# Optimization experiments

Hardware: AMD Instinct MI355X
Metric: run time of the kernel (lower is better)

The kernel has to match this reference:

```python
import jax, jax.numpy as jnp
import numpy as np

B, T, E = 4, 2048, 1024
H, D = 16, 64  # num_heads, head_size; H*D == E


def setup_inputs() -> dict:
    key = jax.random.key(0)
    ks = jax.random.split(key, 8)
    s = 0.02
    x = jax.random.normal(ks[0], (B, T, E), dtype=jnp.float32)
    attention_mask = jnp.ones((B, T), dtype=jnp.float32)
    # stacked per-head projection weights (no bias), torch Linear: y = x @ W.T
    Wq = jax.random.normal(ks[1], (H, E, D), dtype=jnp.float32) * s
    Wk = jax.random.normal(ks[2], (H, E, D), dtype=jnp.float32) * s
    Wv = jax.random.normal(ks[3], (H, E, D), dtype=jnp.float32) * s
    Wo = jax.random.normal(ks[4], (E, E), dtype=jnp.float32) * s
    bo = jnp.zeros((E,), dtype=jnp.float32)
    return {"x": x, "attention_mask": attention_mask, "Wq": Wq, "Wk": Wk,
            "Wv": Wv, "Wo": Wo, "bo": bo}


def reference(x, attention_mask, Wq, Wk, Wv, Wo, bo):
    # per-head projections, vectorized over heads: [B,T,E] x [H,E,D] -> [B,H,T,D]
    q = jnp.einsum('bte,hed->bhtd', x, Wq)
    k = jnp.einsum('bte,hed->bhtd', x, Wk)
    v = jnp.einsum('bte,hed->bhtd', x, Wv)
    scores = jnp.einsum('bhtd,bhsd->bhts', q, k) / jnp.sqrt(jnp.float32(D))
    # causal mask (tril): masked_fill with -inf
    causal = jnp.tril(jnp.ones((T, T), dtype=bool))
    scores = jnp.where(causal[None, None, :, :], scores, -jnp.inf)
    # padding mask: weights += (1 - mask) * finfo(float32).min, broadcast over queries
    neg = jnp.finfo(jnp.float32).min
    scores = scores + ((1.0 - attention_mask) * neg)[:, None, None, :]
    weights = jax.nn.softmax(scores, axis=-1)
    out = jnp.einsum('bhts,bhsd->bthd', weights, v).reshape(B, T, H * D)
    return out @ Wo.T + bo
```

## Files before the change

kernel.cpp:

```cpp
#include <hip/hip_runtime.h>
#include <hip/hip_bf16.h>

#define B_ 4
#define T_ 2048
#define E_ 1024
#define H_ 16
#define D_ 64
#define M_ (B_*T_)

typedef short bf16x8 __attribute__((ext_vector_type(8)));
typedef float f32x4  __attribute__((ext_vector_type(4)));
typedef float f32x16 __attribute__((ext_vector_type(16)));

__device__ __forceinline__ short f2bf(float f) {
    __hip_bfloat16 h = __float2bfloat16(f);
    return *reinterpret_cast<short*>(&h);
}

__device__ __forceinline__ void async_ld16(const void* g, void* l) {
    __builtin_amdgcn_global_load_lds(
        (const __attribute__((address_space(1))) unsigned int*)g,
        (__attribute__((address_space(3))) unsigned int*)l, 16, 0, 0);
}

__global__ __launch_bounds__(256) void prep_fused(
        const float* __restrict__ x,   const float* __restrict__ Wo,
        const float* __restrict__ Wq,  const float* __restrict__ Wk,
        const float* __restrict__ Wv,  const float* __restrict__ mask,
        short* __restrict__ xb, short* __restrict__ Wob,
        short* __restrict__ Wt, float* __restrict__ bias) {
    __shared__ float tile[64][65];
    const int bi  = blockIdx.x;
    const int tid = threadIdx.x;

    if (bi < 9216) {
        const float* src = (bi < 8192) ? x : Wo;
        short* dst       = (bi < 8192) ? xb : Wob;
        const int i = ((bi < 8192) ? bi : (bi - 8192)) * 256 + tid;
        float4 v = ((const float4*)src)[i];
        short4 o = make_short4(f2bf(v.x), f2bf(v.y), f2bf(v.z), f2bf(v.w));
        ((short4*)dst)[i] = o;
    } else if (bi < 9984) {
        const int idx = bi - 9216;
        const int which = idx >> 8;
        const int h  = (idx & 255) >> 4;
        const int e0 = (idx & 15) * 64;
        const float* __restrict__ W = (which == 0) ? Wq : (which == 1) ? Wk : Wv;
#pragma unroll
        for (int r = 0; r < 4; ++r) {
            int lin = tid + r * 256;
            int er = lin >> 4, c4 = (lin & 15) * 4;
            float4 v = *(const float4*)(W + ((size_t)h * E_ + e0 + er) * D_ + c4);
            tile[er][c4 + 0] = v.x; tile[er][c4 + 1] = v.y;
            tile[er][c4 + 2] = v.z; tile[er][c4 + 3] = v.w;
        }
        __syncthreads();
#pragma unroll
        for (int r = 0; r < 4; ++r) {
            int lin = tid + r * 256;
            int dr = lin >> 4, j4 = (lin & 15) * 4;
            short4 o = make_short4(f2bf(tile[j4 + 0][dr]), f2bf(tile[j4 + 1][dr]),
                                   f2bf(tile[j4 + 2][dr]), f2bf(tile[j4 + 3][dr]));
            *(short4*)(Wt + ((size_t)which * 1024 + h * 64 + dr) * E_ + e0 + j4) = o;
        }
    } else {
        const int i = (bi - 9984) * 256 + tid;
        float bm = (1.0f - mask[i]) * -3.402823466e38f;
        bias[i] = fmaf(bm, 1.4426950f, -8.6561700f);
    }
}

template <int MODE>
__global__ __launch_bounds__(512, 4) void mfma_gemm(
        const short* __restrict__ A,
        const short* __restrict__ Bt,
        short* __restrict__ qo, short* __restrict__ ko, short* __restrict__ vo,
        float* __restrict__ Cout, const float* __restrict__ bo) {
    __shared__ __align__(16) char lds[3 * 24576];

    const int tid  = threadIdx.x;
    const int wave = tid >> 6, lane = tid & 63;
    const int c = lane & 15, quad = lane >> 4;
    const int wm = wave >> 1, wn = wave & 1;
    const int m0 = blockIdx.x * 256;
    const int n0 = blockIdx.y * 128;

    const int ar = tid >> 2;
    const int ag = (tid & 3) ^ ((tid >> 3) & 3);

    int aoff[4], boff[4];
#pragma unroll
    for (int mi = 0; mi < 4; ++mi) {
        int row = wm * 64 + mi * 16 + c;
        aoff[mi] = row * 64 + ((quad ^ ((row >> 1) & 3)) << 4);
    }
#pragma unroll
    for (int ni = 0; ni < 4; ++ni) {
        int row = wn * 64 + ni * 16 + c;
        boff[ni] = 16384 + row * 64 + ((quad ^ ((row >> 1) & 3)) << 4);
    }

    f32x4 acc[4][4] = {};

#define STG(bufb, k0v) do {                                                  \
        async_ld16(A  + (size_t)(m0 + ar) * 1024 + (k0v) + ag * 8,           \
                   lds + (bufb) + wave * 1024);                              \
        async_ld16(A  + (size_t)(m0 + 128 + ar) * 1024 + (k0v) + ag * 8,     \
                   lds + (bufb) + 8192 + wave * 1024);                       \
        async_ld16(Bt + (size_t)(n0 + ar) * 1024 + (k0v) + ag * 8,           \
                   lds + (bufb) + 16384 + wave * 1024);                      \
    } while (0)

    STG(0, 0);
    STG(24576, 32);
    asm volatile("s_waitcnt vmcnt(3)" ::: "memory");
    __builtin_amdgcn_s_barrier();

    int rbase = 0;
#pragma unroll 1
    for (int k = 0; k < 32; ++k) {
        const char* rb = lds + rbase;
        const int wbase = (rbase == 0) ? 49152 : rbase - 24576;

        if (k < 30) STG(wbase, (k + 2) * 32);

        bf16x8 a_[4], b_[4];
#pragma unroll
        for (int mi = 0; mi < 4; ++mi)
            a_[mi] = *(const bf16x8*)(rb + aoff[mi]);
#pragma unroll
        for (int ni = 0; ni < 4; ++ni)
            b_[ni] = *(const bf16x8*)(rb + boff[ni]);

        __builtin_amdgcn_s_setprio(1);
#pragma unroll
        for (int mi = 0; mi < 4; ++mi)
#pragma unroll
            for (int ni = 0; ni < 4; ++ni)
                acc[mi][ni] = __builtin_amdgcn_mfma_f32_16x16x32_bf16(
                    a_[mi], b_[ni], acc[mi][ni], 0, 0, 0);
        __builtin_amdgcn_s_setprio(0);

        if (k < 30)       asm volatile("s_waitcnt vmcnt(3)" ::: "memory");
        else if (k == 30) asm volatile("s_waitcnt vmcnt(0)" ::: "memory");
        if (k < 31) __builtin_amdgcn_s_barrier();

        rbase = (rbase == 49152) ? 0 : rbase + 24576;
    }
#undef STG

    if (MODE == 0) {
        const int which = n0 >> 10;
        const int nb = n0 & 1023;
        if (which == 2) {
#pragma unroll
            for (int mi = 0; mi < 4; ++mi) {
                const int m = m0 + wm * 64 + mi * 16 + quad * 4;
                const int b = m >> 11, t = m & 2047;
#pragma unroll
                for (int ni = 0; ni < 4; ++ni) {
                    const int n = nb + wn * 64 + ni * 16 + c;
                    const int h = n >> 6, d = n & 63;
                    short4 s4 = make_short4(f2bf(acc[mi][ni][0]), f2bf(acc[mi][ni][1]),
                                            f2bf(acc[mi][ni][2]), f2bf(acc[mi][ni][3]));
                    *(short4*)(vo + (((size_t)b * H_ + h) * D_ + d) * T_ + t) = s4;
                }
            }
        } else {
            short* __restrict__ outp = (which == 0) ? qo : ko;
            const float sc = (which == 0) ? 0.18033688f : 1.0f;
#pragma unroll
            for (int mi = 0; mi < 4; ++mi) {
#pragma unroll
                for (int i = 0; i < 4; ++i) {
                    const int m = m0 + wm * 64 + mi * 16 + quad * 4 + i;
                    const int b = m >> 11, t = m & 2047;
#pragma unroll
                    for (int ni = 0; ni < 4; ++ni) {
                        const int n = nb + wn * 64 + ni * 16 + c;
                        const int h = n >> 6, d = n & 63;
                        outp[(((size_t)b * H_ + h) * T_ + t) * D_ + d] =
                            f2bf(acc[mi][ni][i] * sc);
                    }
                }
            }
        }
    } else {
#pragma unroll
        for (int mi = 0; mi < 4; ++mi) {
#pragma unroll
            for (int i = 0; i < 4; ++i) {
                const int m = m0 + wm * 64 + mi * 16 + quad * 4 + i;
#pragma unroll
                for (int ni = 0; ni < 4; ++ni) {
                    const int n = n0 + wn * 64 + ni * 16 + c;
                    Cout[(size_t)m * E_ + n] = acc[mi][ni][i] + bo[n];
                }
            }
        }
    }
}

__global__ __launch_bounds__(256, 4) void flash_attn7(
        const short* __restrict__ qg,
        const short* __restrict__ kg,
        const short* __restrict__ vtg,
        const float* __restrict__ biasg,
        short* __restrict__ attn) {
    const int h = blockIdx.x, b = blockIdx.y;
    const int kb = 15 - blockIdx.z;
    const int tid  = threadIdx.x;
    const int wave = tid >> 6, lane = tid & 63;
    const int ln = lane & 31, hi = lane >> 5;
    const int q0w = kb * 128 + wave * 32;
    const int mytile = 4 * kb + wave;
    const int nt = 4 * kb + 4;

    __shared__ __align__(16) char lds[40960];

    const size_t bh = (size_t)b * H_ + h;
    const short* qbh  = qg  + bh * (size_t)T_ * D_;
    const short* kbh  = kg  + bh * (size_t)T_ * D_;
    const short* vtbh = vtg + bh * (size_t)D_ * T_;
    const float* biasb = biasg + (size_t)b * T_;

    const int ks = tid >> 3, kgs = (tid & 7) ^ (ks & 7);
    const int vd = tid >> 2, vgs = ((tid & 3) - (vd >> 1)) & 3;

    int kaddr[4];
#pragma unroll
    for (int kc = 0; kc < 4; ++kc)
        kaddr[kc] = ln * 128 + ((((kc << 1) + hi) ^ (ln & 7)) << 4);
    int vaddr[4];
#pragma unroll
    for (int dh = 0; dh < 2; ++dh)
#pragma unroll
        for (int kc2 = 0; kc2 < 2; ++kc2) {
            int d = dh * 32 + ln;
            vaddr[dh * 2 + kc2] =
                4096 + d * 64 + (((((kc2 << 1) + hi) + (d >> 1)) & 3) << 4);
        }

    bf16x8 qf[4];
#pragma unroll
    for (int kc = 0; kc < 4; ++kc)
        qf[kc] = *(const bf16x8*)(qbh + (size_t)(q0w + ln) * D_ + kc * 16 + hi * 8);

#pragma unroll
    for (int r = 0; r < 2; ++r)
        async_ld16(biasb + r * 1024 + tid * 4,
                   lds + 32768 + r * 4096 + wave * 1024);

#define STAGE_T(tt2) do {                                                   \
        const int _s0 = (tt2) << 5;                                         \
        const int _bb = ((tt2) & 3) * 8192;                                 \
        async_ld16(kbh + (size_t)(_s0 + ks) * D_ + (kgs << 3),              \
                   lds + _bb + wave * 1024);                                \
        async_ld16(vtbh + (size_t)vd * T_ + _s0 + (vgs << 3),               \
                   lds + _bb + 4096 + wave * 1024);                         \
    } while (0)

    STAGE_T(0);
    STAGE_T(1);

    f32x16 O0 = {}, O1 = {};
    float lacc = 0.0f;

    for (int tt = 0; tt < nt; ++tt) {
        if (tt + 2 < nt) STAGE_T(tt + 2);
        const int rem = nt - 1 - tt;
        if (rem >= 2)      asm volatile("s_waitcnt vmcnt(4)" ::: "memory");
        else if (rem == 1) asm volatile("s_waitcnt vmcnt(2)" ::: "memory");
        else               asm volatile("s_waitcnt vmcnt(0)" ::: "memory");
        __builtin_amdgcn_s_barrier();

        if (tt <= mytile) {
            const int s0 = tt << 5;
            const int bb = (tt & 3) * 8192;

            f32x4 b4[4];
#pragma unroll
            for (int g = 0; g < 4; ++g)
                b4[g] = *(const f32x4*)(lds + 32768 + (s0 + g * 8 + hi * 4) * 4);

            f32x16 S = {};
            __builtin_amdgcn_s_setprio(1);
#pragma unroll
            for (int kc = 0; kc < 4; ++kc) {
                bf16x8 ka = *(const bf16x8*)(lds + bb + kaddr[kc]);
                S = __builtin_amdgcn_mfma_f32_32x32x16_bf16(ka, qf[kc], S, 0, 0, 0);
            }
            __builtin_amdgcn_s_setprio(0);

            float p[16];
#pragma unroll
            for (int r = 0; r < 16; ++r) {
                float bb2 = ((const float*)&b4[r >> 2])[r & 3];
                p[r] = __builtin_amdgcn_exp2f(S[r] + bb2);
            }
            if (tt == mytile) {
#pragma unroll
                for (int r = 0; r < 16; ++r)
                    if (((r & 3) + ((r >> 2) << 3) + (hi << 2)) > ln)
                        p[r] = 0.0f;
            }
            {
                float t0 = (p[0] + p[1]) + (p[2] + p[3]);
                float t1 = (p[4] + p[5]) + (p[6] + p[7]);
                float t2s = (p[8] + p[9]) + (p[10] + p[11]);
                float t3 = (p[12] + p[13]) + (p[14] + p[15]);
                lacc += (t0 + t1) + (t2s + t3);
            }

            unsigned int u0, u1, u2, u3, u4, u5, u6, u7;
            asm("v_cvt_pk_bf16_f32 %0, %1, %2" : "=v"(u0) : "v"(p[0]),  "v"(p[1]));
            asm("v_cvt_pk_bf16_f32 %0, %1, %2" : "=v"(u1) : "v"(p[2]),  "v"(p[3]));
            asm("v_cvt_pk_bf16_f32 %0, %1, %2" : "=v"(u2) : "v"(p[4]),  "v"(p[5]));
            asm("v_cvt_pk_bf16_f32 %0, %1, %2" : "=v"(u3) : "v"(p[6]),  "v"(p[7]));
            asm("v_cvt_pk_bf16_f32 %0, %1, %2" : "=v"(u4) : "v"(p[8]),  "v"(p[9]));
            asm("v_cvt_pk_bf16_f32 %0, %1, %2" : "=v"(u5) : "v"(p[10]), "v"(p[11]));
            asm("v_cvt_pk_bf16_f32 %0, %1, %2" : "=v"(u6) : "v"(p[12]), "v"(p[13]));
            asm("v_cvt_pk_bf16_f32 %0, %1, %2" : "=v"(u7) : "v"(p[14]), "v"(p[15]));
            asm("v_permlane32_swap_b32 %0, %1" : "+v"(u0), "+v"(u2));
            asm("v_permlane32_swap_b32 %0, %1" : "+v"(u1), "+v"(u3));
            asm("v_permlane32_swap_b32 %0, %1" : "+v"(u4), "+v"(u6));
            asm("v_permlane32_swap_b32 %0, %1" : "+v"(u5), "+v"(u7));
            union { unsigned int w[4]; bf16x8 v; } pa0, pa1;
            pa0.w[0] = u0; pa0.w[1] = u1; pa0.w[2] = u2; pa0.w[3] = u3;
            pa1.w[0] = u4; pa1.w[1] = u5; pa1.w[2] = u6; pa1.w[3] = u7;

            bf16x8 v00 = *(const bf16x8*)(lds + bb + vaddr[0]);
            bf16x8 v01 = *(const bf16x8*)(lds + bb + vaddr[1]);
            bf16x8 v10 = *(const bf16x8*)(lds + bb + vaddr[2]);
            bf16x8 v11 = *(const bf16x8*)(lds + bb + vaddr[3]);
            __builtin_amdgcn_s_setprio(1);
            O0 = __builtin_amdgcn_mfma_f32_32x32x16_bf16(pa0.v, v00, O0, 0, 0, 0);
            O0 = __builtin_amdgcn_mfma_f32_32x32x16_bf16(pa1.v, v01, O0, 0, 0, 0);
            O1 = __builtin_amdgcn_mfma_f32_32x32x16_bf16(pa0.v, v10, O1, 0, 0, 0);
            O1 = __builtin_amdgcn_mfma_f32_32x32x16_bf16(pa1.v, v11, O1, 0, 0, 0);
            __builtin_amdgcn_s_setprio(0);
        }
    }
#undef STAGE_T

    unsigned int la = __float_as_uint(lacc), lb2 = la;
    asm("v_permlane32_swap_b32 %0, %1" : "+v"(la), "+v"(lb2));
    const float ltot = __uint_as_float(la) + __uint_as_float(lb2);

    __syncthreads();
    float* lsh = (float*)lds + wave * 32;
    if (hi == 0) lsh[ln] = 1.0f / ltot;
    __syncthreads();

    short* ab = attn + (size_t)b * T_ * E_ + h * D_;
#pragma unroll
    for (int r = 0; r < 16; ++r) {
        const int qrow = (r & 3) + ((r >> 2) << 3) + (hi << 2);
        const float iv = lsh[qrow];
        const size_t base = (size_t)(q0w + qrow) * E_;
        ab[base + ln]      = f2bf(O0[r] * iv);
        ab[base + 32 + ln] = f2bf(O1[r] * iv);
    }
}

extern "C" void kernel_launch(void* const* d_in, const int* in_sizes, int n_in,
                              void* d_out, int out_size, void* d_ws, size_t ws_size,
                              hipStream_t stream) {
    const float* x    = (const float*)d_in[0];
    const float* mask = (const float*)d_in[1];
    const float* Wq   = (const float*)d_in[2];
    const float* Wk   = (const float*)d_in[3];
    const float* Wv   = (const float*)d_in[4];
    const float* Wo   = (const float*)d_in[5];
    const float* bo   = (const float*)d_in[6];
    float* out        = (float*)d_out;

    const size_t S = (size_t)M_ * E_;
    char* ws = (char*)d_ws;
    short* xb   = (short*)ws;
    short* qb   = (short*)(ws + S * 2);
    short* kb   = (short*)(ws + S * 4);
    short* vtb  = (short*)(ws + S * 6);
    short* Wt   = (short*)(ws + S * 8);
    short* Wob  = (short*)(ws + S * 8 + (size_t)3 * 1024 * 1024 * 2);
    float* bias = (float*)(ws + S * 8 + (size_t)4 * 1024 * 1024 * 2);
    short* attnb = xb;

    prep_fused<<<dim3(10016), 256, 0, stream>>>(
        x, Wo, Wq, Wk, Wv, mask, xb, Wob, Wt, bias);

    mfma_gemm<0><<<dim3(M_ / 256, 3 * E_ / 128), 512, 0, stream>>>(
        xb, Wt, qb, kb, vtb, nullptr, nullptr);

    flash_attn7<<<dim3(H_, B_, 16), 256, 0, stream>>>(qb, kb, vtb, bias, attnb);

    mfma_gemm<1><<<dim3(M_ / 256, E_ / 128), 512, 0, stream>>>(
        attnb, Wob, nullptr, nullptr, nullptr, out, bo);
}
```

Before: 234.3 us.

## Process attention KV tiles in pairs with one barrier and swizzle GEMM block order

The flash attention loop now handles two 32-key tiles per iteration. It waits on all outstanding loads and takes one barrier per pair, then prefetches the next pair into the other half of the 4-slot ring. This halves the number of barriers and waitcnts, but drops the finer-grained prefetch overlap of the old two-tile-ahead scheme. Separately, the GEMM kernels remap block indices with an 8-way swizzle, spreading consecutive blocks across XCDs/L2 domains to improve cache locality.

```diff
diff --git a/kernel.cpp b/kernel.cpp
--- a/kernel.cpp
+++ b/kernel.cpp
@@ -82,8 +82,12 @@
     const int wave = tid >> 6, lane = tid & 63;
     const int c = lane & 15, quad = lane >> 4;
     const int wm = wave >> 1, wn = wave & 1;
-    const int m0 = blockIdx.x * 256;
-    const int n0 = blockIdx.y * 128;
+
+    const int orig = blockIdx.y * gridDim.x + blockIdx.x;
+    const int cpx  = (gridDim.x * gridDim.y) >> 3;
+    const int swz  = (orig & 7) * cpx + (orig >> 3);
+    const int m0 = (swz & 31) * 256;
+    const int n0 = (swz >> 5) * 128;
 
     const int ar = tid >> 2;
     const int ag = (tid & 3) ^ ((tid >> 3) & 3);
@@ -201,7 +205,81 @@
     }
 }
 
-__global__ __launch_bounds__(256, 4) void flash_attn7(
+__device__ __forceinline__ void attn_tile(
+        const int tt, const int mytile, const char* __restrict__ lds,
+        const int ln, const int hi, const bf16x8* __restrict__ qf,
+        const int4 ka4, const int4 va4,
+        f32x16& O0, f32x16& O1, float& lacc) {
+    if (tt > mytile) return;
+    const int s0 = tt << 5;
+    const int bb = (tt & 3) * 8192;
+    const int ka[4] = {ka4.x, ka4.y, ka4.z, ka4.w};
+    const int va[4] = {va4.x, va4.y, va4.z, va4.w};
+
+    f32x4 b4[4];
+#pragma unroll
+    for (int g = 0; g < 4; ++g)
+        b4[g] = *(const f32x4*)(lds + 32768 + (s0 + g * 8 + hi * 4) * 4);
+
+    f32x16 S = {};
+    __builtin_amdgcn_s_setprio(1);
+#pragma unroll
+    for (int kc = 0; kc < 4; ++kc) {
+        bf16x8 kv = *(const bf16x8*)(lds + bb + ka[kc]);
+        S = __builtin_amdgcn_mfma_f32_32x32x16_bf16(kv, qf[kc], S, 0, 0, 0);
+    }
+    __builtin_amdgcn_s_setprio(0);
+
+    float p[16];
+#pragma unroll
+    for (int r = 0; r < 16; ++r) {
+        float bb2 = ((const float*)&b4[r >> 2])[r & 3];
+        p[r] = __builtin_amdgcn_exp2f(S[r] + bb2);
+    }
+    if (tt == mytile) {
+#pragma unroll
+        for (int r = 0; r < 16; ++r)
+            if (((r & 3) + ((r >> 2) << 3) + (hi << 2)) > ln)
+                p[r] = 0.0f;
+    }
+    {
+        float t0 = (p[0] + p[1]) + (p[2] + p[3]);
+        float t1 = (p[4] + p[5]) + (p[6] + p[7]);
+        float t2s = (p[8] + p[9]) + (p[10] + p[11]);
+        float t3 = (p[12] + p[13]) + (p[14] + p[15]);
+        lacc += (t0 + t1) + (t2s + t3);
+    }
+
+    unsigned int u0, u1, u2, u3, u4, u5, u6, u7;
+    asm("v_cvt_pk_bf16_f32 %0, %1, %2" : "=v"(u0) : "v"(p[0]),  "v"(p[1]));
+    asm("v_cvt_pk_bf16_f32 %0, %1, %2" : "=v"(u1) : "v"(p[2]),  "v"(p[3]));
+    asm("v_cvt_pk_bf16_f32 %0, %1, %2" : "=v"(u2) : "v"(p[4]),  "v"(p[5]));
+    asm("v_cvt_pk_bf16_f32 %0, %1, %2" : "=v"(u3) : "v"(p[6]),  "v"(p[7]));
+    asm("v_cvt_pk_bf16_f32 %0, %1, %2" : "=v"(u4) : "v"(p[8]),  "v"(p[9]));
+    asm("v_cvt_pk_bf16_f32 %0, %1, %2" : "=v"(u5) : "v"(p[10]), "v"(p[11]));
+    asm("v_cvt_pk_bf16_f32 %0, %1, %2" : "=v"(u6) : "v"(p[12]), "v"(p[13]));
+    asm("v_cvt_pk_bf16_f32 %0, %1, %2" : "=v"(u7) : "v"(p[14]), "v"(p[15]));
+    asm("v_permlane32_swap_b32 %0, %1" : "+v"(u0), "+v"(u2));
+    asm("v_permlane32_swap_b32 %0, %1" : "+v"(u1), "+v"(u3));
+    asm("v_permlane32_swap_b32 %0, %1" : "+v"(u4), "+v"(u6));
+    asm("v_permlane32_swap_b32 %0, %1" : "+v"(u5), "+v"(u7));
+    union { unsigned int w[4]; bf16x8 v; } pa0, pa1;
+    pa0.w[0] = u0; pa0.w[1] = u1; pa0.w[2] = u2; pa0.w[3] = u3;
+    pa1.w[0] = u4; pa1.w[1] = u5; pa1.w[2] = u6; pa1.w[3] = u7;
+
+    bf16x8 v00 = *(const bf16x8*)(lds + bb + va[0]);
+    bf16x8 v01 = *(const bf16x8*)(lds + bb + va[1]);
+    bf16x8 v10 = *(const bf16x8*)(lds + bb + va[2]);
+    bf16x8 v11 = *(const bf16x8*)(lds + bb + va[3]);
+    __builtin_amdgcn_s_setprio(1);
+    O0 = __builtin_amdgcn_mfma_f32_32x32x16_bf16(pa0.v, v00, O0, 0, 0, 0);
+    O0 = __builtin_amdgcn_mfma_f32_32x32x16_bf16(pa1.v, v01, O0, 0, 0, 0);
+    O1 = __builtin_amdgcn_mfma_f32_32x32x16_bf16(pa0.v, v10, O1, 0, 0, 0);
+    O1 = __builtin_amdgcn_mfma_f32_32x32x16_bf16(pa1.v, v11, O1, 0, 0, 0);
+    __builtin_amdgcn_s_setprio(0);
+}
+
+__global__ __launch_bounds__(256, 4) void flash_attn8(
         const short* __restrict__ qg,
         const short* __restrict__ kg,
         const short* __restrict__ vtg,
@@ -215,6 +293,7 @@
     const int q0w = kb * 128 + wave * 32;
     const int mytile = 4 * kb + wave;
     const int nt = 4 * kb + 4;
+    const int np = nt >> 1;
 
     __shared__ __align__(16) char lds[40960];
 
@@ -227,19 +306,23 @@
     const int ks = tid >> 3, kgs = (tid & 7) ^ (ks & 7);
     const int vd = tid >> 2, vgs = ((tid & 3) - (vd >> 1)) & 3;
 
-    int kaddr[4];
-#pragma unroll
-    for (int kc = 0; kc < 4; ++kc)
-        kaddr[kc] = ln * 128 + ((((kc << 1) + hi) ^ (ln & 7)) << 4);
-    int vaddr[4];
-#pragma unroll
-    for (int dh = 0; dh < 2; ++dh)
-#pragma unroll
-        for (int kc2 = 0; kc2 < 2; ++kc2) {
-            int d = dh * 32 + ln;
-            vaddr[dh * 2 + kc2] =
-                4096 + d * 64 + (((((kc2 << 1) + hi) + (d >> 1)) & 3) << 4);
-        }
+    int4 ka4, va4;
+    {
+        int tmp[4];
+#pragma unroll
+        for (int kc = 0; kc < 4; ++kc)
+            tmp[kc] = ln * 128 + ((((kc << 1) + hi) ^ (ln & 7)) << 4);
+        ka4 = make_int4(tmp[0], tmp[1], tmp[2], tmp[3]);
+#pragma unroll
+        for (int dh = 0; dh < 2; ++dh)
+#pragma unroll
+            for (int kc2 = 0; kc2 < 2; ++kc2) {
+                int d = dh * 32 + ln;
+                tmp[dh * 2 + kc2] =
+                    4096 + d * 64 + (((((kc2 << 1) + hi) + (d >> 1)) & 3) << 4);
+            }
+        va4 = make_int4(tmp[0], tmp[1], tmp[2], tmp[3]);
+    }
 
     bf16x8 qf[4];
 #pragma unroll
@@ -266,80 +349,14 @@
     f32x16 O0 = {}, O1 = {};
     float lacc = 0.0f;
 
-    for (int tt = 0; tt < nt; ++tt) {
-        if (tt + 2 < nt) STAGE_T(tt + 2);
-        const int rem = nt - 1 - tt;
-        if (rem >= 2)      asm volatile("s_waitcnt vmcnt(4)" ::: "memory");
-        else if (rem == 1) asm volatile("s_waitcnt vmcnt(2)" ::: "memory");
-        else               asm volatile("s_waitcnt vmcnt(0)" ::: "memory");
+#pragma unroll 1
+    for (int j = 0; j < np; ++j) {
+        asm volatile("s_waitcnt vmcnt(0)" ::: "memory");
         __builtin_amdgcn_s_barrier();
-
-        if (tt <= mytile) {
-            const int s0 = tt << 5;
-            const int bb = (tt & 3) * 8192;
-
-            f32x4 b4[4];
-#pragma unroll
-            for (int g = 0; g < 4; ++g)
-                b4[g] = *(const f32x4*)(lds + 32768 + (s0 + g * 8 + hi * 4) * 4);
-
-            f32x16 S = {};
-            __builtin_amdgcn_s_setprio(1);
-#pragma unroll
-            for (int kc = 0; kc < 4; ++kc) {
-                bf16x8 ka = *(const bf16x8*)(lds + bb + kaddr[kc]);
-                S = __builtin_amdgcn_mfma_f32_32x32x16_bf16(ka, qf[kc], S, 0, 0, 0);
-            }
-            __builtin_amdgcn_s_setprio(0);
-
-            float p[16];
-#pragma unroll
-            for (int r = 0; r < 16; ++r) {
-                float bb2 = ((const float*)&b4[r >> 2])[r & 3];
-                p[r] = __builtin_amdgcn_exp2f(S[r] + bb2);
-            }
-            if (tt == mytile) {
-#pragma unroll
-                for (int r = 0; r < 16; ++r)
-                    if (((r & 3) + ((r >> 2) << 3) + (hi << 2)) > ln)
-                        p[r] = 0.0f;
-            }
-            {
-                float t0 = (p[0] + p[1]) + (p[2] + p[3]);
-                float t1 = (p[4] + p[5]) + (p[6] + p[7]);
-                float t2s = (p[8] + p[9]) + (p[10] + p[11]);
-                float t3 = (p[12] + p[13]) + (p[14] + p[15]);
-                lacc += (t0 + t1) + (t2s + t3);
-            }
-
-            unsigned int u0, u1, u2, u3, u4, u5, u6, u7;
-            asm("v_cvt_pk_bf16_f32 %0, %1, %2" : "=v"(u0) : "v"(p[0]),  "v"(p[1]));
-            asm("v_cvt_pk_bf16_f32 %0, %1, %2" : "=v"(u1) : "v"(p[2]),  "v"(p[3]));
-            asm("v_cvt_pk_bf16_f32 %0, %1, %2" : "=v"(u2) : "v"(p[4]),  "v"(p[5]));
-            asm("v_cvt_pk_bf16_f32 %0, %1, %2" : "=v"(u3) : "v"(p[6]),  "v"(p[7]));
-            asm("v_cvt_pk_bf16_f32 %0, %1, %2" : "=v"(u4) : "v"(p[8]),  "v"(p[9]));
-            asm("v_cvt_pk_bf16_f32 %0, %1, %2" : "=v"(u5) : "v"(p[10]), "v"(p[11]));
-            asm("v_cvt_pk_bf16_f32 %0, %1, %2" : "=v"(u6) : "v"(p[12]), "v"(p[13]));
-            asm("v_cvt_pk_bf16_f32 %0, %1, %2" : "=v"(u7) : "v"(p[14]), "v"(p[15]));
-            asm("v_permlane32_swap_b32 %0, %1" : "+v"(u0), "+v"(u2));
-            asm("v_permlane32_swap_b32 %0, %1" : "+v"(u1), "+v"(u3));
-            asm("v_permlane32_swap_b32 %0, %1" : "+v"(u4), "+v"(u6));
-            asm("v_permlane32_swap_b32 %0, %1" : "+v"(u5), "+v"(u7));
-            union { unsigned int w[4]; bf16x8 v; } pa0, pa1;
-            pa0.w[0] = u0; pa0.w[1] = u1; pa0.w[2] = u2; pa0.w[3] = u3;
-            pa1.w[0] = u4; pa1.w[1] = u5; pa1.w[2] = u6; pa1.w[3] = u7;
-
-            bf16x8 v00 = *(const bf16x8*)(lds + bb + vaddr[0]);
-            bf16x8 v01 = *(const bf16x8*)(lds + bb + vaddr[1]);
-            bf16x8 v10 = *(const bf16x8*)(lds + bb + vaddr[2]);
-            bf16x8 v11 = *(const bf16x8*)(lds + bb + vaddr[3]);
-            __builtin_amdgcn_s_setprio(1);
-            O0 = __builtin_amdgcn_mfma_f32_32x32x16_bf16(pa0.v, v00, O0, 0, 0, 0);
-            O0 = __builtin_amdgcn_mfma_f32_32x32x16_bf16(pa1.v, v01, O0, 0, 0, 0);
-            O1 = __builtin_amdgcn_mfma_f32_32x32x16_bf16(pa0.v, v10, O1, 0, 0, 0);
-            O1 = __builtin_amdgcn_mfma_f32_32x32x16_bf16(pa1.v, v11, O1, 0, 0, 0);
-            __builtin_amdgcn_s_setprio(0);
-        }
+        if (j + 1 < np) { STAGE_T(2 * j + 2); STAGE_T(2 * j + 3); }
+
+        attn_tile(2 * j,     mytile, lds, ln, hi, qf, ka4, va4, O0, O1, lacc);
+        attn_tile(2 * j + 1, mytile, lds, ln, hi, qf, ka4, va4, O0, O1, lacc);
     }
 #undef STAGE_T
 
@@ -392,7 +409,7 @@
     mfma_gemm<0><<<dim3(M_ / 256, 3 * E_ / 128), 512, 0, stream>>>(
         xb, Wt, qb, kb, vtb, nullptr, nullptr);
 
-    flash_attn7<<<dim3(H_, B_, 16), 256, 0, stream>>>(qb, kb, vtb, bias, attnb);
+    flash_attn8<<<dim3(H_, B_, 16), 256, 0, stream>>>(qb, kb, vtb, bias, attnb);
 
     mfma_gemm<1><<<dim3(M_ / 256, E_ / 128), 512, 0, stream>>>(
         attnb, Wob, nullptr, nullptr, nullptr, out, bo);
```

New measurement: 251.0 us. +7.1%, slower.
